# Kernel tuning notes

Measured on AMD Instinct MI355X. Metric: run time of the kernel, lower is better.

Reference implementation:

```python
import jax, jax.numpy as jnp
import numpy as np


def setup_inputs() -> dict:
    key = jax.random.key(0)
    ks = jax.random.split(key, 8)
    B, C, H, W = 4, 256, 64, 64
    Ci = C // 8  # inter_channels = 32
    x = jax.random.normal(ks[0], (B, C, H, W), dtype=jnp.float32)
    # 1x1 conv weights stored as [out, in] matrices (kernel size 1)
    sq = 1.0 / np.sqrt(C)
    Wq = jax.random.uniform(ks[1], (Ci, C), jnp.float32, -sq, sq)
    bq = jax.random.uniform(ks[2], (Ci,), jnp.float32, -sq, sq)
    Wk = jax.random.uniform(ks[3], (Ci, C), jnp.float32, -sq, sq)
    bk = jax.random.uniform(ks[4], (Ci,), jnp.float32, -sq, sq)
    Wv = jax.random.uniform(ks[5], (C, C), jnp.float32, -sq, sq)
    bv = jax.random.uniform(ks[6], (C,), jnp.float32, -sq, sq)
    # torch initializes gamma to zeros; use a nonzero value so output depends on attention path
    gamma = jnp.array([0.5], dtype=jnp.float32)
    return {"x": x, "Wq": Wq, "bq": bq, "Wk": Wk, "bk": bk, "Wv": Wv, "bv": bv, "gamma": gamma}


def reference(x, Wq, bq, Wk, bk, Wv, bv, gamma):
    B, C, H, W = x.shape
    N = H * W
    xf = x.reshape(B, C, N)                        # [B, C, N]
    # 1x1 convs == channel-mixing matmuls
    q = jnp.einsum('oc,bcn->bon', Wq, xf) + bq[None, :, None]   # [B, Ci, N]
    k = jnp.einsum('oc,bcn->bon', Wk, xf) + bk[None, :, None]   # [B, Ci, N]
    v = jnp.einsum('oc,bcn->bon', Wv, xf) + bv[None, :, None]   # [B, C,  N]
    # energy[b, n, m] = sum_c q[b, c, n] * k[b, c, m]  (no scaling, per DANet)
    energy = jnp.einsum('bcn,bcm->bnm', q, k)      # [B, N, N]
    attention = jax.nn.softmax(energy, axis=-1)    # softmax over keys m
    # out[b, c, n] = sum_m v[b, c, m] * attention[b, n, m]
    out = jnp.einsum('bcm,bnm->bcn', v, attention)
    out = out.reshape(B, C, H, W)
    return gamma[0] * out + x
```

## Files before the change

### kernel.cpp

```cpp
#include <hip/hip_runtime.h>
#include <hip/hip_bf16.h>
#include <math.h>

typedef __bf16 bf16x8 __attribute__((ext_vector_type(8)));
typedef float  floatx4 __attribute__((ext_vector_type(4)));
typedef float  floatx16 __attribute__((ext_vector_type(16)));
typedef unsigned u32x2 __attribute__((ext_vector_type(2)));

#define MFMA(a, b, c)   __builtin_amdgcn_mfma_f32_16x16x32_bf16((a), (b), (c), 0, 0, 0)
#define MFMA32(a, b, c) __builtin_amdgcn_mfma_f32_32x32x16_bf16((a), (b), (c), 0, 0, 0)

__device__ __forceinline__ unsigned short f2bf(float f) {
  union { float f; unsigned u; } v; v.f = f;
  unsigned r = v.u + 0x7FFFu + ((v.u >> 16) & 1u);
  return (unsigned short)(r >> 16);
}
__device__ __forceinline__ float bf2f(unsigned short u) {
  union { unsigned u; float f; } v; v.u = ((unsigned)u) << 16;
  return v.f;
}
__device__ __forceinline__ unsigned pack2(float a, float b) {
  __bf16 x = (__bf16)a, y = (__bf16)b;
  unsigned short ux = __builtin_bit_cast(unsigned short, x);
  unsigned short uy = __builtin_bit_cast(unsigned short, y);
  return (unsigned)ux | ((unsigned)uy << 16);
}
__device__ __forceinline__ float exp2_fast(float x) {
#if __has_builtin(__builtin_amdgcn_exp2f)
  return __builtin_amdgcn_exp2f(x);
#else
  return exp2f(x);
#endif
}

__global__ __launch_bounds__(256) void k_wconv(const float* __restrict__ Wq,
                                               const float* __restrict__ Wk,
                                               const float* __restrict__ Wv,
                                               unsigned short* __restrict__ Wall) {
  int i = blockIdx.x * 256 + threadIdx.x;
  int o = i >> 8, c = i & 255;
  float v = (o < 32) ? Wq[o * 256 + c]
          : (o < 64) ? Wk[(o - 32) * 256 + c]
                     : Wv[(o - 64) * 256 + c];
  Wall[i] = f2bf(v);
}

__global__ __launch_bounds__(256) void k_projx(const float* __restrict__ x,
                                               const unsigned short* __restrict__ Wall,
                                               const float* __restrict__ bq,
                                               const float* __restrict__ bk,
                                               const float* __restrict__ bv,
                                               unsigned short* __restrict__ qbf,
                                               unsigned short* __restrict__ kbf,
                                               unsigned short* __restrict__ vbf) {
  int b = blockIdx.x >> 8;
  int m0 = (blockIdx.x & 255) * 16;
  int tid = threadIdx.x;
  int qr = tid >> 6;
  int lane = tid & 63;
  int l15 = lane & 15, quad = lane >> 4;

  __shared__ alignas(16) unsigned short xs[16][264];
  __shared__ alignas(16) unsigned short Os[4][64][24];

  {
    const float* xrow = x + ((size_t)b * 256 + tid) * 4096 + m0;
#pragma unroll
    for (int g = 0; g < 4; ++g) {
      float4 d = *(const float4*)(xrow + g * 4);
      xs[g * 4 + 0][tid] = f2bf(d.x);
      xs[g * 4 + 1][tid] = f2bf(d.y);
      xs[g * 4 + 2][tid] = f2bf(d.z);
      xs[g * 4 + 3][tid] = f2bf(d.w);
    }
  }
  __syncthreads();

  floatx4 acc[5];
#pragma unroll
  for (int tt = 0; tt < 5; ++tt) acc[tt] = floatx4{0.f, 0.f, 0.f, 0.f};

#pragma unroll
  for (int ks = 0; ks < 8; ++ks) {
    bf16x8 a = *(const bf16x8*)&xs[l15][ks * 32 + quad * 8];
    {
      bf16x8 w = *(const bf16x8*)(Wall + (size_t)(qr * 16 + l15) * 256 + ks * 32 + quad * 8);
      acc[0] = MFMA(a, w, acc[0]);
    }
#pragma unroll
    for (int t = 0; t < 4; ++t) {
      int gt = 4 + qr * 4 + t;
      bf16x8 w = *(const bf16x8*)(Wall + (size_t)(gt * 16 + l15) * 256 + ks * 32 + quad * 8);
      acc[1 + t] = MFMA(a, w, acc[1 + t]);
    }
  }
  {
    int o = qr * 16 + l15;
    float bias = (o < 32) ? bq[o] : bk[o - 32];
    float scale = (o < 32) ? 1.44269504088896340736f : 1.0f;
    unsigned short* dst = (o < 32) ? qbf : kbf;
    int oc = o & 31;
    int kh = oc >> 4, h2 = (oc >> 3) & 1, c8 = oc & 7;
#pragma unroll
    for (int r = 0; r < 4; ++r) {
      int m = m0 + quad * 4 + r;
      dst[(size_t)b * 131072 + (size_t)(m >> 5) * 1024 + kh * 512 + h2 * 256 +
          (m & 31) * 8 + c8] = f2bf((acc[0][r] + bias) * scale);
    }
  }
#pragma unroll
  for (int t = 0; t < 4; ++t) {
    int lr = t * 16 + l15;
    int c = qr * 64 + lr;
    float bias = bv[c];
#pragma unroll
    for (int r = 0; r < 4; ++r)
      Os[qr][lr][quad * 4 + r] = f2bf(acc[1 + t][r] + bias);
  }
  __syncthreads();
  {
    int kb = m0 >> 5, kk = (m0 >> 4) & 1;
#pragma unroll
    for (int i = 0; i < 2; ++i) {
      int idx = lane + 64 * i;
      int r = idx >> 1, g = idx & 1;
      int c = qr * 64 + r;
      int cb = c >> 5, ch = c & 31;
      *(uint4*)(vbf + (size_t)b * 1048576 + (size_t)kb * 8192 +
                (size_t)cb * 1024 + kk * 512 + g * 256 + ch * 8) =
          *(const uint4*)&Os[qr][r][g * 8];
    }
  }
}

__device__ __forceinline__ void softmax_pack(floatx16 st, float& lp, bf16x8 (&pa)[2], int hi) {
  float p[16];
#pragma unroll
  for (int r = 0; r < 16; ++r) p[r] = exp2_fast(st[r]);
  lp += (((p[0] + p[1]) + (p[2] + p[3])) + ((p[4] + p[5]) + (p[6] + p[7]))) +
        (((p[8] + p[9]) + (p[10] + p[11])) + ((p[12] + p[13]) + (p[14] + p[15])));
  unsigned d0[4], d1[4];
#pragma unroll
  for (int t = 0; t < 4; ++t) {
    d0[t] = pack2(p[4 * t + 0], p[4 * t + 1]);
    d1[t] = pack2(p[4 * t + 2], p[4 * t + 3]);
  }
#pragma unroll
  for (int ks = 0; ks < 2; ++ks) {
#if __has_builtin(__builtin_amdgcn_permlane32_swap)
    (void)hi;
    u32x2 r0 = __builtin_amdgcn_permlane32_swap(d0[2 * ks], d0[2 * ks + 1], false, false);
    u32x2 r1 = __builtin_amdgcn_permlane32_swap(d1[2 * ks], d1[2 * ks + 1], false, false);
    union { unsigned u[4]; bf16x8 v; } u;
    u.u[0] = r0[0]; u.u[1] = r1[0]; u.u[2] = r0[1]; u.u[3] = r1[1];
    pa[ks] = u.v;
#else
    unsigned s0 = hi ? d0[2 * ks] : d0[2 * ks + 1];
    unsigned s1 = hi ? d1[2 * ks] : d1[2 * ks + 1];
    unsigned o0 = (unsigned)__shfl_xor((int)s0, 32);
    unsigned o1 = (unsigned)__shfl_xor((int)s1, 32);
    union { unsigned u[4]; bf16x8 v; } u;
    u.u[0] = hi ? o0 : d0[2 * ks];
    u.u[1] = hi ? o1 : d1[2 * ks];
    u.u[2] = hi ? d0[2 * ks + 1] : o0;
    u.u[3] = hi ? d1[2 * ks + 1] : o1;
    pa[ks] = u.v;
#endif
  }
}

__global__ __launch_bounds__(64, 2) void k_attn(const unsigned short* __restrict__ qbf,
                                                const unsigned short* __restrict__ kbf,
                                                const unsigned short* __restrict__ vbf,
                                                unsigned short* __restrict__ Obf,
                                                float* __restrict__ lsum) {
  int wg = (blockIdx.x & 7) * 256 + (blockIdx.x >> 3);
  const int qb = wg & 63;
  const int g  = wg >> 6;
  const int cw = g & 1;
  const int s  = (g >> 1) & 3;
  const int b  = g >> 3;
  const int lane = threadIdx.x & 63;
  const int l31 = lane & 31;
  const int hi  = lane >> 5;
  const int q0  = qb * 64;

  const floatx16 z16 = {0.f, 0.f, 0.f, 0.f, 0.f, 0.f, 0.f, 0.f,
                        0.f, 0.f, 0.f, 0.f, 0.f, 0.f, 0.f, 0.f};

  bf16x8 qf[2][2];
  {
    const unsigned short* qbase =
        qbf + (size_t)b * 131072 + (size_t)(qb * 2) * 1024 + hi * 256 + l31 * 8;
#pragma unroll
    for (int qs2 = 0; qs2 < 2; ++qs2)
#pragma unroll
      for (int kh = 0; kh < 2; ++kh)
        qf[qs2][kh] = *(const bf16x8*)(qbase + qs2 * 1024 + kh * 512);
  }

  floatx16 acc[2][4];
#pragma unroll
  for (int i = 0; i < 2; ++i)
#pragma unroll
    for (int j = 0; j < 4; ++j) acc[i][j] = z16;

  float lp0 = 0.f, lp1 = 0.f;

  const unsigned short* krow =
      kbf + (size_t)b * 131072 + (size_t)(s * 32) * 1024 + hi * 256 + l31 * 8;
  const unsigned short* vrow =
      vbf + (size_t)b * 1048576 + (size_t)(s * 32) * 8192 + (size_t)(cw * 4) * 1024 +
      hi * 256 + l31 * 8;

  bf16x8 kf0 = *(const bf16x8*)krow;
  bf16x8 kf1 = *(const bf16x8*)(krow + 512);
  floatx16 st0 = MFMA32(kf0, qf[0][0], z16);
  st0 = MFMA32(kf1, qf[0][1], st0);
  floatx16 st1 = MFMA32(kf0, qf[1][0], z16);
  st1 = MFMA32(kf1, qf[1][1], st1);
  kf0 = *(const bf16x8*)(krow + 1024);
  kf1 = *(const bf16x8*)(krow + 1024 + 512);

  for (int it = 0; it < 32; ++it) {
    bf16x8 vb[4][2];
    const unsigned short* vit = vrow + (size_t)it * 8192;
#pragma unroll
    for (int ct = 0; ct < 4; ++ct) {
      vb[ct][0] = *(const bf16x8*)(vit + ct * 1024);
      vb[ct][1] = *(const bf16x8*)(vit + ct * 1024 + 512);
    }

    bf16x8 pa[2][2];
    softmax_pack(st0, lp0, pa[0], hi);
    softmax_pack(st1, lp1, pa[1], hi);

    st0 = MFMA32(kf0, qf[0][0], z16);
    st0 = MFMA32(kf1, qf[0][1], st0);
    st1 = MFMA32(kf0, qf[1][0], z16);
    st1 = MFMA32(kf1, qf[1][1], st1);

    const unsigned short* kn = krow + (size_t)((it + 2) & 31) * 1024;
    kf0 = *(const bf16x8*)kn;
    kf1 = *(const bf16x8*)(kn + 512);

    __builtin_amdgcn_s_setprio(1);
#pragma unroll
    for (int ct = 0; ct < 4; ++ct) {
      acc[0][ct] = MFMA32(pa[0][0], vb[ct][0], acc[0][ct]);
      acc[1][ct] = MFMA32(pa[1][0], vb[ct][0], acc[1][ct]);
      acc[0][ct] = MFMA32(pa[0][1], vb[ct][1], acc[0][ct]);
      acc[1][ct] = MFMA32(pa[1][1], vb[ct][1], acc[1][ct]);
    }
    __builtin_amdgcn_s_setprio(0);
  }

  lp0 += __shfl_xor(lp0, 32);
  lp1 += __shfl_xor(lp1, 32);
  if (cw == 0) {
    float lv = hi ? lp1 : lp0;
    lsum[((size_t)s * 4 + b) * 4096 + q0 + hi * 32 + l31] = lv;
  }
#pragma unroll
  for (int qs2 = 0; qs2 < 2; ++qs2)
#pragma unroll
    for (int ct = 0; ct < 4; ++ct) {
      unsigned short* orow = Obf +
          (((size_t)s * 4 + b) * 256 + cw * 128 + ct * 32 + l31) * 4096 +
          q0 + qs2 * 32 + hi * 4;
#pragma unroll
      for (int gi = 0; gi < 4; ++gi) {
        unsigned w0 = pack2(acc[qs2][ct][4 * gi + 0], acc[qs2][ct][4 * gi + 1]);
        unsigned w1 = pack2(acc[qs2][ct][4 * gi + 2], acc[qs2][ct][4 * gi + 3]);
        unsigned long long w = (unsigned long long)w0 | ((unsigned long long)w1 << 32);
        *(unsigned long long*)(orow + 8 * gi) = w;
      }
    }
}

__global__ __launch_bounds__(256) void k_merge(const unsigned short* __restrict__ Obf,
                                               const float* __restrict__ lsum,
                                               const float* __restrict__ x,
                                               const float* __restrict__ gma,
                                               float* __restrict__ out) {
  int t = blockIdx.x * 256 + threadIdx.x;
  int n4 = t & 1023;
  int c = (t >> 10) & 255;
  int b = t >> 18;
  int n = n4 << 2;
  size_t xa = (((size_t)b * 256 + c) << 12) + n;
  float4 xv = *(const float4*)(x + xa);
  float L0 = 0.f, L1 = 0.f, L2 = 0.f, L3 = 0.f;
  float o0 = 0.f, o1 = 0.f, o2 = 0.f, o3 = 0.f;
#pragma unroll
  for (int s = 0; s < 4; ++s) {
    float4 ls = *(const float4*)(lsum + (((size_t)s * 4 + b) << 12) + n);
    L0 += ls.x; L1 += ls.y; L2 += ls.z; L3 += ls.w;
    ushort4 ov = *(const ushort4*)(Obf + ((((size_t)s * 4 + b) * 256 + c) << 12) + n);
    o0 += bf2f(ov.x); o1 += bf2f(ov.y); o2 += bf2f(ov.z); o3 += bf2f(ov.w);
  }
  float g = gma[0];
  float4 r;
  r.x = xv.x + g * o0 / L0;
  r.y = xv.y + g * o1 / L1;
  r.z = xv.z + g * o2 / L2;
  r.w = xv.w + g * o3 / L3;
  *(float4*)(out + xa) = r;
}

extern "C" void kernel_launch(void* const* d_in, const int* in_sizes, int n_in,
                              void* d_out, int out_size, void* d_ws, size_t ws_size,
                              hipStream_t stream) {
  const float* x   = (const float*)d_in[0];
  const float* Wq  = (const float*)d_in[1];
  const float* bq  = (const float*)d_in[2];
  const float* Wk  = (const float*)d_in[3];
  const float* bk  = (const float*)d_in[4];
  const float* Wv  = (const float*)d_in[5];
  const float* bv  = (const float*)d_in[6];
  const float* gma = (const float*)d_in[7];
  float* out = (float*)d_out;

  unsigned short* qbf  = (unsigned short*)d_ws;
  unsigned short* kbf  = qbf + (size_t)4 * 131072;
  unsigned short* vbf  = kbf + (size_t)4 * 131072;
  unsigned short* Wall = vbf + (size_t)4 * 1048576;
  unsigned short* Obf  = Wall + (size_t)320 * 256;
  float* lsum = (float*)(Obf + (size_t)4 * 4 * 256 * 4096);

  k_wconv<<<320, 256, 0, stream>>>(Wq, Wk, Wv, Wall);
  k_projx<<<1024, 256, 0, stream>>>(x, Wall, bq, bk, bv, qbf, kbf, vbf);
  k_attn<<<2048, 64, 0, stream>>>(qbf, kbf, vbf, Obf, lsum);
  k_merge<<<4096, 256, 0, stream>>>(Obf, lsum, x, gma, out);
}
```

Before: 168.7 us.

## Double-buffer V tiles in LDS via async global-to-LDS loads

V tiles for the PV matmul are no longer loaded straight into registers at the top of each iteration. They are now streamed into a double-buffered LDS array with global_load_lds, one iteration ahead, and read back with ds reads just before the MFMAs. A manual vmcnt wait keeps only the newest prefetch and the K loads outstanding. The aim is to hide global-memory latency for V behind the softmax and QK MFMAs and to cut register pressure from the 8 bf16x8 V fragments. In exchange the kernel uses 16 KB of LDS per single-wave block and depends on a hand-counted waitcnt for correctness.

```diff
diff --git a/kernel.cpp b/kernel.cpp
--- a/kernel.cpp
+++ b/kernel.cpp
@@ -169,6 +169,21 @@
   }
 }
 
+__device__ __forceinline__ void stage_v(const unsigned short* src,
+                                        unsigned short* dst, int lane) {
+#pragma unroll
+  for (int i = 0; i < 8; ++i) {
+#if __has_builtin(__builtin_amdgcn_global_load_lds)
+    __builtin_amdgcn_global_load_lds(
+        (const __attribute__((address_space(1))) unsigned int*)(src + i * 512 + lane * 8),
+        (__attribute__((address_space(3))) unsigned int*)(dst + i * 512),
+        16, 0, 0);
+#else
+    *(uint4*)(dst + i * 512 + (size_t)lane * 8) = *(const uint4*)(src + i * 512 + lane * 8);
+#endif
+  }
+}
+
 __global__ __launch_bounds__(64, 2) void k_attn(const unsigned short* __restrict__ qbf,
                                                 const unsigned short* __restrict__ kbf,
                                                 const unsigned short* __restrict__ vbf,
@@ -185,6 +200,8 @@
   const int hi  = lane >> 5;
   const int q0  = qb * 64;
 
+  __shared__ alignas(16) unsigned short Vl[2][4096];
+
   const floatx16 z16 = {0.f, 0.f, 0.f, 0.f, 0.f, 0.f, 0.f, 0.f,
                         0.f, 0.f, 0.f, 0.f, 0.f, 0.f, 0.f, 0.f};
 
@@ -209,10 +226,11 @@
 
   const unsigned short* krow =
       kbf + (size_t)b * 131072 + (size_t)(s * 32) * 1024 + hi * 256 + l31 * 8;
-  const unsigned short* vrow =
-      vbf + (size_t)b * 1048576 + (size_t)(s * 32) * 8192 + (size_t)(cw * 4) * 1024 +
-      hi * 256 + l31 * 8;
-
+  const unsigned short* vtile =
+      vbf + (size_t)b * 1048576 + (size_t)(s * 32) * 8192 + (size_t)(cw * 4) * 1024;
+  const int ldsfrag = hi * 256 + l31 * 8;
+
+  stage_v(vtile, &Vl[0][0], lane);
   bf16x8 kf0 = *(const bf16x8*)krow;
   bf16x8 kf1 = *(const bf16x8*)(krow + 512);
   floatx16 st0 = MFMA32(kf0, qf[0][0], z16);
@@ -223,13 +241,7 @@
   kf1 = *(const bf16x8*)(krow + 1024 + 512);
 
   for (int it = 0; it < 32; ++it) {
-    bf16x8 vb[4][2];
-    const unsigned short* vit = vrow + (size_t)it * 8192;
-#pragma unroll
-    for (int ct = 0; ct < 4; ++ct) {
-      vb[ct][0] = *(const bf16x8*)(vit + ct * 1024);
-      vb[ct][1] = *(const bf16x8*)(vit + ct * 1024 + 512);
-    }
+    stage_v(vtile + (size_t)((it + 1) & 31) * 8192, &Vl[(it + 1) & 1][0], lane);
 
     bf16x8 pa[2][2];
     softmax_pack(st0, lp0, pa[0], hi);
@@ -244,13 +256,18 @@
     kf0 = *(const bf16x8*)kn;
     kf1 = *(const bf16x8*)(kn + 512);
 
+    asm volatile("s_waitcnt vmcnt(10)" ::: "memory");
+
+    const unsigned short* Vb = &Vl[it & 1][0];
     __builtin_amdgcn_s_setprio(1);
 #pragma unroll
     for (int ct = 0; ct < 4; ++ct) {
-      acc[0][ct] = MFMA32(pa[0][0], vb[ct][0], acc[0][ct]);
-      acc[1][ct] = MFMA32(pa[1][0], vb[ct][0], acc[1][ct]);
-      acc[0][ct] = MFMA32(pa[0][1], vb[ct][1], acc[0][ct]);
-      acc[1][ct] = MFMA32(pa[1][1], vb[ct][1], acc[1][ct]);
+      bf16x8 v0 = *(const bf16x8*)(Vb + ct * 1024 + ldsfrag);
+      bf16x8 v1 = *(const bf16x8*)(Vb + ct * 1024 + 512 + ldsfrag);
+      acc[0][ct] = MFMA32(pa[0][0], v0, acc[0][ct]);
+      acc[1][ct] = MFMA32(pa[1][0], v0, acc[1][ct]);
+      acc[0][ct] = MFMA32(pa[0][1], v1, acc[0][ct]);
+      acc[1][ct] = MFMA32(pa[1][1], v1, acc[1][ct]);
     }
     __builtin_amdgcn_s_setprio(0);
   }
```

Result: slower. 173.3 us (+2.8%).

## Repartition attention work: 32-query tiles covering all 256 channels per wave

Applied to the files above, without the earlier changes.

Each attention workgroup now handles 32 queries across all 256 value channels, where before it handled 64 queries over half the channels. This removes the duplicated QK^T and softmax work that the two channel halves each repeated. The partial output buffer is relaid out as per-query-block tiles, and the merge kernel's indexing is updated to match. In exchange, each wave loads twice as many V fragments per iteration for a single softmax tile, and the one-step-ahead overlap of the score MFMA with the PV MFMAs is dropped.

```diff
diff --git a/kernel.cpp b/kernel.cpp
--- a/kernel.cpp
+++ b/kernel.cpp
@@ -175,107 +175,84 @@
                                                 unsigned short* __restrict__ Obf,
                                                 float* __restrict__ lsum) {
   int wg = (blockIdx.x & 7) * 256 + (blockIdx.x >> 3);
-  const int qb = wg & 63;
-  const int g  = wg >> 6;
-  const int cw = g & 1;
-  const int s  = (g >> 1) & 3;
-  const int b  = g >> 3;
+  const int qb = wg & 127;
+  const int g  = wg >> 7;
+  const int s  = g & 3;
+  const int b  = g >> 2;
   const int lane = threadIdx.x & 63;
   const int l31 = lane & 31;
   const int hi  = lane >> 5;
-  const int q0  = qb * 64;
+  const int q0  = qb * 32;
 
   const floatx16 z16 = {0.f, 0.f, 0.f, 0.f, 0.f, 0.f, 0.f, 0.f,
                         0.f, 0.f, 0.f, 0.f, 0.f, 0.f, 0.f, 0.f};
 
-  bf16x8 qf[2][2];
+  bf16x8 qf[2];
   {
     const unsigned short* qbase =
-        qbf + (size_t)b * 131072 + (size_t)(qb * 2) * 1024 + hi * 256 + l31 * 8;
-#pragma unroll
-    for (int qs2 = 0; qs2 < 2; ++qs2)
-#pragma unroll
-      for (int kh = 0; kh < 2; ++kh)
-        qf[qs2][kh] = *(const bf16x8*)(qbase + qs2 * 1024 + kh * 512);
-  }
-
-  floatx16 acc[2][4];
-#pragma unroll
-  for (int i = 0; i < 2; ++i)
-#pragma unroll
-    for (int j = 0; j < 4; ++j) acc[i][j] = z16;
-
-  float lp0 = 0.f, lp1 = 0.f;
+        qbf + (size_t)b * 131072 + (size_t)qb * 1024 + hi * 256 + l31 * 8;
+    qf[0] = *(const bf16x8*)(qbase);
+    qf[1] = *(const bf16x8*)(qbase + 512);
+  }
+
+  floatx16 acc[8];
+#pragma unroll
+  for (int j = 0; j < 8; ++j) acc[j] = z16;
+
+  float lp = 0.f;
 
   const unsigned short* krow =
       kbf + (size_t)b * 131072 + (size_t)(s * 32) * 1024 + hi * 256 + l31 * 8;
   const unsigned short* vrow =
-      vbf + (size_t)b * 1048576 + (size_t)(s * 32) * 8192 + (size_t)(cw * 4) * 1024 +
-      hi * 256 + l31 * 8;
+      vbf + (size_t)b * 1048576 + (size_t)(s * 32) * 8192 + hi * 256 + l31 * 8;
 
   bf16x8 kf0 = *(const bf16x8*)krow;
   bf16x8 kf1 = *(const bf16x8*)(krow + 512);
-  floatx16 st0 = MFMA32(kf0, qf[0][0], z16);
-  st0 = MFMA32(kf1, qf[0][1], st0);
-  floatx16 st1 = MFMA32(kf0, qf[1][0], z16);
-  st1 = MFMA32(kf1, qf[1][1], st1);
-  kf0 = *(const bf16x8*)(krow + 1024);
-  kf1 = *(const bf16x8*)(krow + 1024 + 512);
 
   for (int it = 0; it < 32; ++it) {
-    bf16x8 vb[4][2];
+    bf16x8 vb[8][2];
     const unsigned short* vit = vrow + (size_t)it * 8192;
 #pragma unroll
-    for (int ct = 0; ct < 4; ++ct) {
-      vb[ct][0] = *(const bf16x8*)(vit + ct * 1024);
-      vb[ct][1] = *(const bf16x8*)(vit + ct * 1024 + 512);
-    }
-
-    bf16x8 pa[2][2];
-    softmax_pack(st0, lp0, pa[0], hi);
-    softmax_pack(st1, lp1, pa[1], hi);
-
-    st0 = MFMA32(kf0, qf[0][0], z16);
-    st0 = MFMA32(kf1, qf[0][1], st0);
-    st1 = MFMA32(kf0, qf[1][0], z16);
-    st1 = MFMA32(kf1, qf[1][1], st1);
-
-    const unsigned short* kn = krow + (size_t)((it + 2) & 31) * 1024;
+    for (int cb = 0; cb < 8; ++cb) {
+      vb[cb][0] = *(const bf16x8*)(vit + cb * 1024);
+      vb[cb][1] = *(const bf16x8*)(vit + cb * 1024 + 512);
+    }
+
+    floatx16 st = MFMA32(kf0, qf[0], z16);
+    st = MFMA32(kf1, qf[1], st);
+
+    const unsigned short* kn = krow + (size_t)((it + 1) & 31) * 1024;
     kf0 = *(const bf16x8*)kn;
     kf1 = *(const bf16x8*)(kn + 512);
 
+    bf16x8 pa[2];
+    softmax_pack(st, lp, pa, hi);
+
     __builtin_amdgcn_s_setprio(1);
 #pragma unroll
-    for (int ct = 0; ct < 4; ++ct) {
-      acc[0][ct] = MFMA32(pa[0][0], vb[ct][0], acc[0][ct]);
-      acc[1][ct] = MFMA32(pa[1][0], vb[ct][0], acc[1][ct]);
-      acc[0][ct] = MFMA32(pa[0][1], vb[ct][1], acc[0][ct]);
-      acc[1][ct] = MFMA32(pa[1][1], vb[ct][1], acc[1][ct]);
+    for (int cb = 0; cb < 8; ++cb) {
+      acc[cb] = MFMA32(pa[0], vb[cb][0], acc[cb]);
+      acc[cb] = MFMA32(pa[1], vb[cb][1], acc[cb]);
     }
     __builtin_amdgcn_s_setprio(0);
   }
 
-  lp0 += __shfl_xor(lp0, 32);
-  lp1 += __shfl_xor(lp1, 32);
-  if (cw == 0) {
-    float lv = hi ? lp1 : lp0;
-    lsum[((size_t)s * 4 + b) * 4096 + q0 + hi * 32 + l31] = lv;
-  }
-#pragma unroll
-  for (int qs2 = 0; qs2 < 2; ++qs2)
-#pragma unroll
-    for (int ct = 0; ct < 4; ++ct) {
-      unsigned short* orow = Obf +
-          (((size_t)s * 4 + b) * 256 + cw * 128 + ct * 32 + l31) * 4096 +
-          q0 + qs2 * 32 + hi * 4;
-#pragma unroll
-      for (int gi = 0; gi < 4; ++gi) {
-        unsigned w0 = pack2(acc[qs2][ct][4 * gi + 0], acc[qs2][ct][4 * gi + 1]);
-        unsigned w1 = pack2(acc[qs2][ct][4 * gi + 2], acc[qs2][ct][4 * gi + 3]);
-        unsigned long long w = (unsigned long long)w0 | ((unsigned long long)w1 << 32);
-        *(unsigned long long*)(orow + 8 * gi) = w;
-      }
-    }
+  lp += __shfl_xor(lp, 32);
+  if (hi == 0) {
+    lsum[((size_t)s * 4 + b) * 4096 + q0 + l31] = lp;
+  }
+#pragma unroll
+  for (int cb = 0; cb < 8; ++cb) {
+    unsigned short* orow = Obf +
+        ((((size_t)s * 4 + b) * 128 + qb) * 256 + cb * 32 + l31) * 32 + hi * 4;
+#pragma unroll
+    for (int gi = 0; gi < 4; ++gi) {
+      unsigned w0 = pack2(acc[cb][4 * gi + 0], acc[cb][4 * gi + 1]);
+      unsigned w1 = pack2(acc[cb][4 * gi + 2], acc[cb][4 * gi + 3]);
+      unsigned long long w = (unsigned long long)w0 | ((unsigned long long)w1 << 32);
+      *(unsigned long long*)(orow + 8 * gi) = w;
+    }
+  }
 }
 
 __global__ __launch_bounds__(256) void k_merge(const unsigned short* __restrict__ Obf,
@@ -288,6 +265,7 @@
   int c = (t >> 10) & 255;
   int b = t >> 18;
   int n = n4 << 2;
+  int qb = n >> 5, off = n & 31;
   size_t xa = (((size_t)b * 256 + c) << 12) + n;
   float4 xv = *(const float4*)(x + xa);
   float L0 = 0.f, L1 = 0.f, L2 = 0.f, L3 = 0.f;
@@ -296,7 +274,8 @@
   for (int s = 0; s < 4; ++s) {
     float4 ls = *(const float4*)(lsum + (((size_t)s * 4 + b) << 12) + n);
     L0 += ls.x; L1 += ls.y; L2 += ls.z; L3 += ls.w;
-    ushort4 ov = *(const ushort4*)(Obf + ((((size_t)s * 4 + b) * 256 + c) << 12) + n);
+    ushort4 ov = *(const ushort4*)(
+        Obf + ((((size_t)s * 4 + b) * 128 + qb) * 256 + c) * 32 + off);
     o0 += bf2f(ov.x); o1 += bf2f(ov.y); o2 += bf2f(ov.z); o3 += bf2f(ov.w);
   }
   float g = gma[0];
```

Result: slower. 180.1 us (+6.8%).

## Fuse split-key merge into attention kernel via shared-memory reduction

Applied to the files above, without the earlier changes.

Each workgroup now holds the four key-split waves for one query block and channel half, and reduces their partial outputs and softmax denominators in LDS. The residual add and gamma scaling happen in the same kernel, so the separate merge kernel is gone. This removes the global round trip of the bf16 partial outputs and the partial sums (16 MB of partials written and read back). In exchange it adds block-wide barriers and LDS use, and it cuts the grid from 2048 single-wave blocks to 512 four-wave blocks, which may hurt scheduling flexibility and occupancy.

```diff
diff --git a/kernel.cpp b/kernel.cpp
--- a/kernel.cpp
+++ b/kernel.cpp
@@ -169,21 +169,26 @@
   }
 }
 
-__global__ __launch_bounds__(64, 2) void k_attn(const unsigned short* __restrict__ qbf,
-                                                const unsigned short* __restrict__ kbf,
-                                                const unsigned short* __restrict__ vbf,
-                                                unsigned short* __restrict__ Obf,
-                                                float* __restrict__ lsum) {
-  int wg = (blockIdx.x & 7) * 256 + (blockIdx.x >> 3);
+__global__ __launch_bounds__(256, 2) void k_attn(const unsigned short* __restrict__ qbf,
+                                                 const unsigned short* __restrict__ kbf,
+                                                 const unsigned short* __restrict__ vbf,
+                                                 const float* __restrict__ x,
+                                                 const float* __restrict__ gma,
+                                                 float* __restrict__ out) {
+  int wg = (blockIdx.x & 7) * 64 + (blockIdx.x >> 3);
   const int qb = wg & 63;
   const int g  = wg >> 6;
   const int cw = g & 1;
-  const int s  = (g >> 1) & 3;
-  const int b  = g >> 3;
+  const int b  = g >> 1;
+  const int s  = threadIdx.x >> 6;
   const int lane = threadIdx.x & 63;
   const int l31 = lane & 31;
   const int hi  = lane >> 5;
   const int q0  = qb * 64;
+
+  __shared__ float lpL[4][64];
+  __shared__ float ltot[64];
+  __shared__ alignas(16) unsigned short Ol[4][128][40];
 
   const floatx16 z16 = {0.f, 0.f, 0.f, 0.f, 0.f, 0.f, 0.f, 0.f,
                         0.f, 0.f, 0.f, 0.f, 0.f, 0.f, 0.f, 0.f};
@@ -257,55 +262,61 @@
 
   lp0 += __shfl_xor(lp0, 32);
   lp1 += __shfl_xor(lp1, 32);
-  if (cw == 0) {
-    float lv = hi ? lp1 : lp0;
-    lsum[((size_t)s * 4 + b) * 4096 + q0 + hi * 32 + l31] = lv;
-  }
-#pragma unroll
-  for (int qs2 = 0; qs2 < 2; ++qs2)
+  lpL[s][hi * 32 + l31] = hi ? lp1 : lp0;
+  __syncthreads();
+  if (threadIdx.x < 64) {
+    int q = threadIdx.x;
+    ltot[q] = (lpL[0][q] + lpL[1][q]) + (lpL[2][q] + lpL[3][q]);
+  }
+  const float gv = gma[0];
+
+#pragma unroll
+  for (int qs2 = 0; qs2 < 2; ++qs2) {
 #pragma unroll
     for (int ct = 0; ct < 4; ++ct) {
-      unsigned short* orow = Obf +
-          (((size_t)s * 4 + b) * 256 + cw * 128 + ct * 32 + l31) * 4096 +
-          q0 + qs2 * 32 + hi * 4;
 #pragma unroll
       for (int gi = 0; gi < 4; ++gi) {
         unsigned w0 = pack2(acc[qs2][ct][4 * gi + 0], acc[qs2][ct][4 * gi + 1]);
         unsigned w1 = pack2(acc[qs2][ct][4 * gi + 2], acc[qs2][ct][4 * gi + 3]);
         unsigned long long w = (unsigned long long)w0 | ((unsigned long long)w1 << 32);
-        *(unsigned long long*)(orow + 8 * gi) = w;
+        *(unsigned long long*)&Ol[s][ct * 32 + l31][8 * gi + 4 * hi] = w;
       }
     }
-}
-
-__global__ __launch_bounds__(256) void k_merge(const unsigned short* __restrict__ Obf,
-                                               const float* __restrict__ lsum,
-                                               const float* __restrict__ x,
-                                               const float* __restrict__ gma,
-                                               float* __restrict__ out) {
-  int t = blockIdx.x * 256 + threadIdx.x;
-  int n4 = t & 1023;
-  int c = (t >> 10) & 255;
-  int b = t >> 18;
-  int n = n4 << 2;
-  size_t xa = (((size_t)b * 256 + c) << 12) + n;
-  float4 xv = *(const float4*)(x + xa);
-  float L0 = 0.f, L1 = 0.f, L2 = 0.f, L3 = 0.f;
-  float o0 = 0.f, o1 = 0.f, o2 = 0.f, o3 = 0.f;
-#pragma unroll
-  for (int s = 0; s < 4; ++s) {
-    float4 ls = *(const float4*)(lsum + (((size_t)s * 4 + b) << 12) + n);
-    L0 += ls.x; L1 += ls.y; L2 += ls.z; L3 += ls.w;
-    ushort4 ov = *(const ushort4*)(Obf + ((((size_t)s * 4 + b) * 256 + c) << 12) + n);
-    o0 += bf2f(ov.x); o1 += bf2f(ov.y); o2 += bf2f(ov.z); o3 += bf2f(ov.w);
-  }
-  float g = gma[0];
-  float4 r;
-  r.x = xv.x + g * o0 / L0;
-  r.y = xv.y + g * o1 / L1;
-  r.z = xv.z + g * o2 / L2;
-  r.w = xv.w + g * o3 / L3;
-  *(float4*)(out + xa) = r;
+    __syncthreads();
+    {
+      int ch = threadIdx.x >> 1;
+      int qh = threadIdx.x & 1;
+      int qoff = qs2 * 32 + qh * 16;
+      float o[16];
+#pragma unroll
+      for (int j = 0; j < 16; ++j) o[j] = 0.f;
+#pragma unroll
+      for (int sp = 0; sp < 4; ++sp) {
+        const uint4* p = (const uint4*)&Ol[sp][ch][qh * 16];
+        uint4 a0 = p[0], a1 = p[1];
+        unsigned uu[8] = {a0.x, a0.y, a0.z, a0.w, a1.x, a1.y, a1.z, a1.w};
+#pragma unroll
+        for (int jj = 0; jj < 8; ++jj) {
+          o[2 * jj + 0] += bf2f((unsigned short)(uu[jj] & 0xffffu));
+          o[2 * jj + 1] += bf2f((unsigned short)(uu[jj] >> 16));
+        }
+      }
+      size_t rowa = ((size_t)b * 256 + cw * 128 + ch) * 4096 + q0 + qoff;
+      const float* xrow = x + rowa;
+      float* orow = out + rowa;
+#pragma unroll
+      for (int j4 = 0; j4 < 4; ++j4) {
+        float4 xv = *(const float4*)(xrow + j4 * 4);
+        float4 r;
+        r.x = xv.x + gv * o[j4 * 4 + 0] / ltot[qoff + j4 * 4 + 0];
+        r.y = xv.y + gv * o[j4 * 4 + 1] / ltot[qoff + j4 * 4 + 1];
+        r.z = xv.z + gv * o[j4 * 4 + 2] / ltot[qoff + j4 * 4 + 2];
+        r.w = xv.w + gv * o[j4 * 4 + 3] / ltot[qoff + j4 * 4 + 3];
+        *(float4*)(orow + j4 * 4) = r;
+      }
+    }
+    __syncthreads();
+  }
 }
 
 extern "C" void kernel_launch(void* const* d_in, const int* in_sizes, int n_in,
@@ -325,11 +336,8 @@
   unsigned short* kbf  = qbf + (size_t)4 * 131072;
   unsigned short* vbf  = kbf + (size_t)4 * 131072;
   unsigned short* Wall = vbf + (size_t)4 * 1048576;
-  unsigned short* Obf  = Wall + (size_t)320 * 256;
-  float* lsum = (float*)(Obf + (size_t)4 * 4 * 256 * 4096);
 
   k_wconv<<<320, 256, 0, stream>>>(Wq, Wk, Wv, Wall);
   k_projx<<<1024, 256, 0, stream>>>(x, Wall, bq, bk, bv, qbf, kbf, vbf);
-  k_attn<<<2048, 64, 0, stream>>>(qbf, kbf, vbf, Obf, lsum);
-  k_merge<<<4096, 256, 0, stream>>>(Obf, lsum, x, gma, out);
-}
+  k_attn<<<512, 256, 0, stream>>>(qbf, kbf, vbf, x, gma, out);
+}
```

Result: faster. 157.2 us (-6.8%).
